# Performance work log

Measured on AMD Instinct MI355X. Metric: run time of the kernel, lower is better.

Reference implementation:

```python
import jax, jax.numpy as jnp
import numpy as np

DIM, HEADS, WH, WW, NPROMPT, NW, BATCH = 384, 12, 7, 7, 5, 64, 32
N = WH * WW + NPROMPT  # 54


def _make_rel_index():
    ch, cw = np.meshgrid(np.arange(WH), np.arange(WW), indexing='ij')
    coords = np.stack([ch, cw]).reshape(2, -1)  # [2, 49]
    rel = coords[:, :, None] - coords[:, None, :]  # [2,49,49]
    rel = rel.transpose(1, 2, 0)
    rel[:, :, 0] += WH - 1
    rel[:, :, 1] += WW - 1
    rel[:, :, 0] *= 2 * WW - 1
    return rel.sum(-1).astype(np.int32)  # [49,49]


def setup_inputs() -> dict:
    key = jax.random.key(0)
    ks = jax.random.split(key, 7)
    B_ = BATCH * NW
    x = jax.random.normal(ks[0], (B_, N, DIM), jnp.float32)
    # 0/-inf style shifted-window mask; random floats exercise the same math
    mask = jnp.where(jax.random.uniform(ks[1], (NW, WH * WW, WH * WW)) > 0.8,
                     jnp.float32(-100.0), jnp.float32(0.0))
    qkv_w = 0.02 * jax.random.normal(ks[2], (3 * DIM, DIM), jnp.float32)
    qkv_b = 0.02 * jax.random.normal(ks[3], (3 * DIM,), jnp.float32)
    proj_w = 0.02 * jax.random.normal(ks[4], (DIM, DIM), jnp.float32)
    proj_b = 0.02 * jax.random.normal(ks[5], (DIM,), jnp.float32)
    rpb_table = 0.02 * jax.random.normal(ks[6], ((2 * WH - 1) * (2 * WW - 1), HEADS), jnp.float32)
    rel_index = jnp.asarray(_make_rel_index())
    return {"x": x, "mask": mask, "qkv_w": qkv_w, "qkv_b": qkv_b,
            "proj_w": proj_w, "proj_b": proj_b, "rpb_table": rpb_table,
            "rel_index": rel_index}


def reference(x, mask, qkv_w, qkv_b, proj_w, proj_b, rpb_table, rel_index):
    B_, n, C = x.shape
    hd = C // HEADS
    scale = hd ** -0.5
    qkv = (x @ qkv_w.T + qkv_b).reshape(B_, n, 3, HEADS, hd)
    qkv = jnp.moveaxis(qkv, 2, 0)  # [3, B_, n, H, hd]
    q, k, v = qkv[0], qkv[1], qkv[2]  # [B_, n, H, hd]
    attn = jnp.einsum('bnhd,bmhd->bhnm', q * scale, k)  # [B_, H, n, n]
    nw2 = WH * WW
    bias = rpb_table[rel_index.reshape(-1)].reshape(nw2, nw2, HEADS)
    bias = jnp.transpose(bias, (2, 0, 1))  # [H, 49, 49]
    bias = jnp.pad(bias, ((0, 0), (NPROMPT, 0), (NPROMPT, 0)))  # [H, n, n]
    attn = attn + bias[None]
    nW = mask.shape[0]
    mask_p = jnp.pad(mask, ((0, 0), (NPROMPT, 0), (NPROMPT, 0)))  # [nW, n, n]
    attn = attn.reshape(B_ // nW, nW, HEADS, n, n) + mask_p[None, :, None]
    attn = jax.nn.softmax(attn.reshape(B_, HEADS, n, n), axis=-1)
    out = jnp.einsum('bhnm,bmhd->bnhd', attn, v).reshape(B_, n, C)
    return out @ proj_w.T + proj_b
```

## Files before the change

kernel.cpp:

```cpp
#include <hip/hip_runtime.h>

#define DIM 384
#define NH 12
#define NT 54
#define NWIN 64
#define MTOT 110592
#define HS ((size_t)MTOT * 32)

typedef __attribute__((ext_vector_type(8))) short short8;
typedef __attribute__((ext_vector_type(4))) float f32x4;

__device__ __forceinline__ unsigned short f2bf(float f) {
  unsigned int u = __float_as_uint(f);
  u += 0x7fffu + ((u >> 16) & 1u);
  return (unsigned short)(u >> 16);
}
__device__ __forceinline__ float bf2f(unsigned short s) {
  return __uint_as_float((unsigned int)s << 16);
}
__device__ __forceinline__ unsigned int cvtpk(float a, float b) {
  unsigned int r;
  asm("v_cvt_pk_bf16_f32 %0, %1, %2" : "=v"(r) : "v"(a), "v"(b));
  return r;
}

__global__ __launch_bounds__(256) void prep2_kernel(
    const float* __restrict__ qkv_w, const float* __restrict__ proj_w,
    const float* __restrict__ mask, const float* __restrict__ rpb,
    const int* __restrict__ rel,
    unsigned short* __restrict__ Wq, unsigned short* __restrict__ Wp,
    unsigned short* __restrict__ bmt) {
  int idx = blockIdx.x * 256 + threadIdx.x;
  if (idx < 1152 * 384) { Wq[idx] = f2bf(qkv_w[idx]); return; }
  idx -= 1152 * 384;
  if (idx < 384 * 384) { Wp[idx] = f2bf(proj_w[idx]); return; }
  idx -= 384 * 384;
  if (idx < NWIN * NH * 64 * 64) {
    int w = idx / (NH * 4096);
    int rem = idx - w * (NH * 4096);
    int h = rem >> 12, r = (rem >> 6) & 63, c = rem & 63;
    float v;
    if (r >= NT || c >= NT) v = -1e30f;
    else if (r >= 5 && c >= 5)
      v = rpb[rel[(r - 5) * 49 + (c - 5)] * NH + h] +
          mask[w * 2401 + (r - 5) * 49 + (c - 5)];
    else v = 0.0f;
    bmt[w * (NH * 4096) + (h << 12) + (c << 6) + r] = f2bf(v);
  }
}

__global__ __launch_bounds__(256) void qkv_gemm4(
    const float* __restrict__ x, const unsigned short* __restrict__ Wq,
    const float* __restrict__ qkv_b,
    unsigned short* __restrict__ Qb, unsigned short* __restrict__ Kb,
    unsigned short* __restrict__ Vb) {
  __shared__ unsigned short As[128][72];
  __shared__ unsigned short Bs[128][72];
  const int s = blockIdx.x;
  const int xcd = s & 7, slot = s >> 3;
  const size_t m0 = (size_t)(xcd * 108 + slot / 9) * 128;
  const int n0 = (slot % 9) * 128;
  const int tid = threadIdx.x;
  const int wv = tid >> 6, ln = tid & 63, g = ln >> 4, lc = ln & 15;
  const int wr = (wv >> 1) * 64, wc = (wv & 1) * 64;
  const int srow = tid >> 3, l8 = tid & 7;

  float4 xa[4], xc[4];
  short8 brg[4];
  f32x4 acc[4][4];
#pragma unroll
  for (int i = 0; i < 4; ++i)
#pragma unroll
    for (int j = 0; j < 4; ++j) acc[i][j] = (f32x4){0.f, 0.f, 0.f, 0.f};

#define QKV_ISSUE(kc_) do {                                              \
    const int k0_ = (kc_) * 64;                                          \
    _Pragma("unroll")                                                    \
    for (int it = 0; it < 4; ++it) {                                     \
      const int r_ = srow + it * 32;                                     \
      const float* ap_ = &x[(m0 + r_) * 384 + k0_ + l8 * 8];             \
      xa[it] = *(const float4*)ap_;                                      \
      xc[it] = *(const float4*)(ap_ + 4);                                \
      brg[it] = *(const short8*)&Wq[(size_t)(n0 + r_) * 384 + k0_ + l8 * 8]; \
    } } while (0)

#define QKV_WRITE() do {                                                 \
    _Pragma("unroll")                                                    \
    for (int it = 0; it < 4; ++it) {                                     \
      const int r_ = srow + it * 32;                                     \
      uint4 u_;                                                          \
      u_.x = cvtpk(xa[it].x, xa[it].y);                                  \
      u_.y = cvtpk(xa[it].z, xa[it].w);                                  \
      u_.z = cvtpk(xc[it].x, xc[it].y);                                  \
      u_.w = cvtpk(xc[it].z, xc[it].w);                                  \
      *(uint4*)&As[r_][l8 * 8] = u_;                                     \
      *(short8*)&Bs[r_][l8 * 8] = brg[it];                               \
    } } while (0)

  QKV_ISSUE(0);
#pragma unroll
  for (int kc = 0; kc < 6; ++kc) {
    if (kc) __syncthreads();
    QKV_WRITE();
    __syncthreads();
    if (kc < 5) QKV_ISSUE(kc + 1);
#pragma unroll
    for (int kk = 0; kk < 2; ++kk) {
      short8 af[4], bfv[4];
#pragma unroll
      for (int ms = 0; ms < 4; ++ms)
        af[ms] = *(const short8*)&As[wr + ms * 16 + lc][kk * 32 + g * 8];
#pragma unroll
      for (int ns = 0; ns < 4; ++ns)
        bfv[ns] = *(const short8*)&Bs[wc + ns * 16 + lc][kk * 32 + g * 8];
#pragma unroll
      for (int ms = 0; ms < 4; ++ms)
#pragma unroll
        for (int ns = 0; ns < 4; ++ns)
          acc[ms][ns] = __builtin_amdgcn_mfma_f32_16x16x32_bf16(
              af[ms], bfv[ns], acc[ms][ns], 0, 0, 0);
    }
  }
#undef QKV_ISSUE
#undef QKV_WRITE

  const int sel = n0 / 384;
  const float factor = (sel == 0) ? 0.17677669529663687f : 1.0f;
  unsigned short* outp = (sel == 0) ? Qb : (sel == 1 ? Kb : Vb);
#pragma unroll
  for (int ns = 0; ns < 4; ++ns) {
    const int n = n0 + wc + ns * 16 + lc;
    const int rl = n - sel * 384;
    const int h = rl >> 5, d = rl & 31;
    const float bias = qkv_b[n];
#pragma unroll
    for (int ms = 0; ms < 4; ++ms) {
      const size_t mrow = m0 + wr + ms * 16 + g * 4;
      const float v0 = (acc[ms][ns][0] + bias) * factor;
      const float v1 = (acc[ms][ns][1] + bias) * factor;
      const float v2 = (acc[ms][ns][2] + bias) * factor;
      const float v3 = (acc[ms][ns][3] + bias) * factor;
      const unsigned int u01 = cvtpk(v0, v1);
      const unsigned int u23 = cvtpk(v2, v3);
      unsigned short* p = &outp[(size_t)h * HS + mrow * 32 + d];
      p[0]  = (unsigned short)(u01 & 0xffffu);
      p[32] = (unsigned short)(u01 >> 16);
      p[64] = (unsigned short)(u23 & 0xffffu);
      p[96] = (unsigned short)(u23 >> 16);
    }
  }
}

__global__ __launch_bounds__(256) void attn2_kernel(
    unsigned short* __restrict__ Qb, const unsigned short* __restrict__ Kb,
    const unsigned short* __restrict__ Vb, const unsigned short* __restrict__ bmt) {
  __shared__ unsigned short Ps[NT][72];
  __shared__ unsigned short vT[32][72];
  const int s = blockIdx.x;
  const int xcd = s & 7, r3 = s >> 3;
  const int h = r3 % 12;
  const int t2 = r3 / 12;
  const int batch = t2 & 31;
  const int w = xcd * 8 + (t2 >> 5);
  const int b = batch * 64 + w;
  const int tid = threadIdx.x;
  const int wv = tid >> 6, ln = tid & 63, g = ln >> 4, lc = ln & 15;
  const int m0 = wv * 16;
  const size_t base = (size_t)b * NT;
  const int arow = (m0 + lc < NT) ? (m0 + lc) : (NT - 1);
  unsigned short* Qh = Qb + (size_t)h * HS;
  const unsigned short* Kh = Kb + (size_t)h * HS;
  const unsigned short* Vh = Vb + (size_t)h * HS;

  for (int i = tid; i < 320; i += 256) {
    int d = i / 10, m = NT + (i - d * 10);
    vT[d][m] = 0;
  }

  const int vr = tid >> 2, vc = (tid & 3) * 8;
  short8 vv;
  if (tid < 216)
    vv = *(const short8*)&Vh[(base + vr) * 32 + vc];

  short8 a = *(const short8*)&Qh[(base + arow) * 32 + g * 8];
  const unsigned short* bmh = &bmt[(size_t)(w * NH + h) << 12];
  const int row0 = m0 + g * 4;
  f32x4 sac[4];
#pragma unroll
  for (int t = 0; t < 4; ++t) {
    const int col = t * 16 + lc;
    const int kr = (col < NT) ? col : (NT - 1);
    short8 kb = *(const short8*)&Kh[(base + kr) * 32 + g * 8];
    uint2 uu = *(const uint2*)&bmh[(col << 6) + row0];
    f32x4 c0;
    c0[0] = bf2f((unsigned short)(uu.x & 0xffffu));
    c0[1] = bf2f((unsigned short)(uu.x >> 16));
    c0[2] = bf2f((unsigned short)(uu.y & 0xffffu));
    c0[3] = bf2f((unsigned short)(uu.y >> 16));
    sac[t] = __builtin_amdgcn_mfma_f32_16x16x32_bf16(a, kb, c0, 0, 0, 0);
  }
  float rmax[4] = {-3.0e38f, -3.0e38f, -3.0e38f, -3.0e38f};
#pragma unroll
  for (int t = 0; t < 4; ++t)
#pragma unroll
    for (int rr = 0; rr < 4; ++rr) rmax[rr] = fmaxf(rmax[rr], sac[t][rr]);
#pragma unroll
  for (int rr = 0; rr < 4; ++rr)
#pragma unroll
    for (int off = 1; off < 16; off <<= 1)
      rmax[rr] = fmaxf(rmax[rr], __shfl_xor(rmax[rr], off));
  float rsum[4] = {0.f, 0.f, 0.f, 0.f};
#pragma unroll
  for (int t = 0; t < 4; ++t)
#pragma unroll
    for (int rr = 0; rr < 4; ++rr) {
      float p = __expf(sac[t][rr] - rmax[rr]);
      sac[t][rr] = p;
      rsum[rr] += p;
    }
#pragma unroll
  for (int rr = 0; rr < 4; ++rr) {
#pragma unroll
    for (int off = 1; off < 16; off <<= 1)
      rsum[rr] += __shfl_xor(rsum[rr], off);
    rsum[rr] = 1.0f / rsum[rr];
  }
#pragma unroll
  for (int t = 0; t < 4; ++t) {
    const int col = t * 16 + lc;
    const unsigned int u01 = cvtpk(sac[t][0] * rsum[0], sac[t][1] * rsum[1]);
    const unsigned int u23 = cvtpk(sac[t][2] * rsum[2], sac[t][3] * rsum[3]);
    if (row0 < NT)     Ps[row0][col]     = (unsigned short)(u01 & 0xffffu);
    if (row0 + 1 < NT) Ps[row0 + 1][col] = (unsigned short)(u01 >> 16);
    if (row0 + 2 < NT) Ps[row0 + 2][col] = (unsigned short)(u23 & 0xffffu);
    if (row0 + 3 < NT) Ps[row0 + 3][col] = (unsigned short)(u23 >> 16);
  }
  if (tid < 216) {
#pragma unroll
    for (int j = 0; j < 8; ++j) vT[vc + j][vr] = (unsigned short)vv[j];
  }
  __syncthreads();
  f32x4 oac[2];
  oac[0] = (f32x4){0.f, 0.f, 0.f, 0.f};
  oac[1] = (f32x4){0.f, 0.f, 0.f, 0.f};
#pragma unroll
  for (int k2 = 0; k2 < 2; ++k2) {
    short8 pa = *(const short8*)&Ps[arow][k2 * 32 + g * 8];
#pragma unroll
    for (int tn = 0; tn < 2; ++tn) {
      short8 vb = *(const short8*)&vT[tn * 16 + lc][k2 * 32 + g * 8];
      oac[tn] = __builtin_amdgcn_mfma_f32_16x16x32_bf16(pa, vb, oac[tn], 0, 0, 0);
    }
  }
#pragma unroll
  for (int tn = 0; tn < 2; ++tn) {
    const int d = tn * 16 + lc;
    const unsigned int u01 = cvtpk(oac[tn][0], oac[tn][1]);
    const unsigned int u23 = cvtpk(oac[tn][2], oac[tn][3]);
    unsigned short* p = &Qh[(base + row0) * 32 + d];
    if (row0 < NT)     p[0]  = (unsigned short)(u01 & 0xffffu);
    if (row0 + 1 < NT) p[32] = (unsigned short)(u01 >> 16);
    if (row0 + 2 < NT) p[64] = (unsigned short)(u23 & 0xffffu);
    if (row0 + 3 < NT) p[96] = (unsigned short)(u23 >> 16);
  }
}

__global__ __launch_bounds__(256) void proj_hmajor(
    const unsigned short* __restrict__ AO, const unsigned short* __restrict__ Wp,
    const float* __restrict__ proj_b, float* __restrict__ out) {
  __shared__ unsigned short As[128][72];
  __shared__ unsigned short Bs[128][72];
  const int s = blockIdx.x;
  const int xcd = s & 7, slot = s >> 3;
  const size_t m0 = (size_t)(xcd * 108 + slot / 3) * 128;
  const int n0 = (slot % 3) * 128;
  const int tid = threadIdx.x;
  const int wv = tid >> 6, ln = tid & 63, g = ln >> 4, lc = ln & 15;
  const int wr = (wv >> 1) * 64, wc = (wv & 1) * 64;
  const int srow = tid >> 3, l8 = tid & 7;

  short8 arg[4], brg[4];
  f32x4 acc[4][4];
#pragma unroll
  for (int i = 0; i < 4; ++i)
#pragma unroll
    for (int j = 0; j < 4; ++j) acc[i][j] = (f32x4){0.f, 0.f, 0.f, 0.f};

#define PRJ_ISSUE(kc_) do {                                              \
    const int kg_ = (kc_) * 64 + l8 * 8;                                 \
    const int hh_ = kg_ >> 5, dd_ = kg_ & 31;                            \
    _Pragma("unroll")                                                    \
    for (int it = 0; it < 4; ++it) {                                     \
      const int r_ = srow + it * 32;                                     \
      arg[it] = *(const short8*)&AO[(size_t)hh_ * HS + (m0 + r_) * 32 + dd_]; \
      brg[it] = *(const short8*)&Wp[(size_t)(n0 + r_) * 384 + kg_];      \
    } } while (0)

#define PRJ_WRITE() do {                                                 \
    _Pragma("unroll")                                                    \
    for (int it = 0; it < 4; ++it) {                                     \
      const int r_ = srow + it * 32;                                     \
      *(short8*)&As[r_][l8 * 8] = arg[it];                               \
      *(short8*)&Bs[r_][l8 * 8] = brg[it];                               \
    } } while (0)

  PRJ_ISSUE(0);
#pragma unroll
  for (int kc = 0; kc < 6; ++kc) {
    if (kc) __syncthreads();
    PRJ_WRITE();
    __syncthreads();
    if (kc < 5) PRJ_ISSUE(kc + 1);
#pragma unroll
    for (int kk = 0; kk < 2; ++kk) {
      short8 af[4], bfv[4];
#pragma unroll
      for (int ms = 0; ms < 4; ++ms)
        af[ms] = *(const short8*)&As[wr + ms * 16 + lc][kk * 32 + g * 8];
#pragma unroll
      for (int ns = 0; ns < 4; ++ns)
        bfv[ns] = *(const short8*)&Bs[wc + ns * 16 + lc][kk * 32 + g * 8];
#pragma unroll
      for (int ms = 0; ms < 4; ++ms)
#pragma unroll
        for (int ns = 0; ns < 4; ++ns)
          acc[ms][ns] = __builtin_amdgcn_mfma_f32_16x16x32_bf16(
              af[ms], bfv[ns], acc[ms][ns], 0, 0, 0);
    }
  }
#undef PRJ_ISSUE
#undef PRJ_WRITE

#pragma unroll
  for (int ns = 0; ns < 4; ++ns) {
    const int n = n0 + wc + ns * 16 + lc;
    const float pb = proj_b[n];
#pragma unroll
    for (int ms = 0; ms < 4; ++ms)
#pragma unroll
      for (int rr = 0; rr < 4; ++rr) {
        const size_t m = m0 + wr + ms * 16 + g * 4 + rr;
        out[m * 384 + n] = acc[ms][ns][rr] + pb;
      }
  }
}

__global__ __launch_bounds__(256) void prep_kernel(
    const float* __restrict__ qkv_w, const float* __restrict__ proj_w,
    const float* __restrict__ mask, const float* __restrict__ rpb,
    const int* __restrict__ rel,
    unsigned short* __restrict__ Wq, unsigned short* __restrict__ Wp,
    float* __restrict__ bias_tab, float* __restrict__ maskp) {
  int idx = blockIdx.x * 256 + threadIdx.x;
  if (idx < 1152 * 384) { Wq[idx] = f2bf(qkv_w[idx]); return; }
  idx -= 1152 * 384;
  if (idx < 384 * 384) { Wp[idx] = f2bf(proj_w[idx]); return; }
  idx -= 384 * 384;
  if (idx < NH * 64 * 64) {
    int h = idx >> 12, r = (idx >> 6) & 63, c = idx & 63;
    float v;
    if (r >= NT || c >= NT) v = -1e30f;
    else if (r >= 5 && c >= 5) v = rpb[rel[(r - 5) * 49 + (c - 5)] * NH + h];
    else v = 0.0f;
    bias_tab[idx] = v;
    return;
  }
  idx -= NH * 64 * 64;
  if (idx < NWIN * 64 * 64) {
    int w = idx >> 12, r = (idx >> 6) & 63, c = idx & 63;
    float v = 0.0f;
    if (r >= 5 && r < NT && c >= 5 && c < NT)
      v = mask[w * 2401 + (r - 5) * 49 + (c - 5)];
    maskp[idx] = v;
  }
}

__global__ __launch_bounds__(256) void fused_attn(
    const float* __restrict__ x, const unsigned short* __restrict__ Wq,
    const float* __restrict__ qkv_b, const float* __restrict__ bias_tab,
    const float* __restrict__ maskp, unsigned short* __restrict__ AO) {
  __shared__ unsigned short xs[NT][392];
  __shared__ unsigned short qs[NT][40];
  __shared__ unsigned short ksm[NT][40];
  __shared__ unsigned short vT[32][72];
  __shared__ unsigned short Ps[NT][72];
  const int b = blockIdx.x;
  const int tid = threadIdx.x;
  const int wv = tid >> 6, ln = tid & 63;
  const int g = ln >> 4, lc = ln & 15;
  const int m0 = wv * 16;
  const int wi = b & 63;
  const float scale = 0.17677669529663687f;
  const float* xb = x + (size_t)b * (NT * DIM);
  for (int i = tid; i < NT * DIM / 4; i += 256) {
    float4 v = ((const float4*)xb)[i];
    int e = i * 4, r = e / DIM, c = e - r * DIM;
    unsigned short* p = &xs[r][c];
    p[0] = f2bf(v.x); p[1] = f2bf(v.y); p[2] = f2bf(v.z); p[3] = f2bf(v.w);
  }
  __syncthreads();
  const int arow = (m0 + lc < NT) ? (m0 + lc) : (NT - 1);
  for (int h = 0; h < NH; ++h) {
    f32x4 acc[6];
#pragma unroll
    for (int t = 0; t < 6; ++t) acc[t] = (f32x4){0.f, 0.f, 0.f, 0.f};
#pragma unroll 2
    for (int kk = 0; kk < 12; ++kk) {
      short8 a = *(const short8*)&xs[arow][kk * 32 + g * 8];
#pragma unroll
      for (int t = 0; t < 6; ++t) {
        const int sel = t >> 1;
        const int wrow = sel * 384 + h * 32 + (t & 1) * 16 + lc;
        short8 bfr = *(const short8*)&Wq[wrow * 384 + kk * 32 + g * 8];
        acc[t] = __builtin_amdgcn_mfma_f32_16x16x32_bf16(a, bfr, acc[t], 0, 0, 0);
      }
    }
#pragma unroll
    for (int t = 0; t < 6; ++t) {
      const int sel = t >> 1;
      const int d = (t & 1) * 16 + lc;
      const float bias = qkv_b[sel * 384 + h * 32 + d];
#pragma unroll
      for (int r = 0; r < 4; ++r) {
        const int m = m0 + g * 4 + r;
        float v = acc[t][r] + bias;
        if (sel == 2) vT[d][m] = f2bf(v);
        else if (m < NT) {
          if (sel == 0) qs[m][d] = f2bf(v * scale);
          else ksm[m][d] = f2bf(v);
        }
      }
    }
    __syncthreads();
    f32x4 sac[4];
    {
      short8 a = *(const short8*)&qs[arow][g * 8];
#pragma unroll
      for (int t = 0; t < 4; ++t) {
        const int kr = (t * 16 + lc < NT) ? (t * 16 + lc) : (NT - 1);
        short8 bfr = *(const short8*)&ksm[kr][g * 8];
        sac[t] = __builtin_amdgcn_mfma_f32_16x16x32_bf16(
            a, bfr, (f32x4){0.f, 0.f, 0.f, 0.f}, 0, 0, 0);
      }
    }
    const float* bt = bias_tab + h * 4096;
    const float* mp = maskp + wi * 4096;
    float sv[4][4];
    float rmax[4];
#pragma unroll
    for (int r = 0; r < 4; ++r) rmax[r] = -3.0e38f;
#pragma unroll
    for (int t = 0; t < 4; ++t) {
      const int col = t * 16 + lc;
#pragma unroll
      for (int r = 0; r < 4; ++r) {
        const int row = m0 + g * 4 + r;
        float s = sac[t][r] + bt[row * 64 + col] + mp[row * 64 + col];
        sv[t][r] = s;
        rmax[r] = fmaxf(rmax[r], s);
      }
    }
#pragma unroll
    for (int r = 0; r < 4; ++r)
#pragma unroll
      for (int off = 1; off < 16; off <<= 1)
        rmax[r] = fmaxf(rmax[r], __shfl_xor(rmax[r], off));
    float rsum[4] = {0.f, 0.f, 0.f, 0.f};
#pragma unroll
    for (int t = 0; t < 4; ++t)
#pragma unroll
      for (int r = 0; r < 4; ++r) {
        float p = __expf(sv[t][r] - rmax[r]);
        sv[t][r] = p;
        rsum[r] += p;
      }
#pragma unroll
    for (int r = 0; r < 4; ++r) {
#pragma unroll
      for (int off = 1; off < 16; off <<= 1)
        rsum[r] += __shfl_xor(rsum[r], off);
      rsum[r] = 1.0f / rsum[r];
    }
#pragma unroll
    for (int t = 0; t < 4; ++t) {
      const int col = t * 16 + lc;
#pragma unroll
      for (int r = 0; r < 4; ++r) {
        const int row = m0 + g * 4 + r;
        if (row < NT) Ps[row][col] = f2bf(sv[t][r] * rsum[r]);
      }
    }
    __syncthreads();
    f32x4 oac[2];
    oac[0] = (f32x4){0.f, 0.f, 0.f, 0.f};
    oac[1] = (f32x4){0.f, 0.f, 0.f, 0.f};
#pragma unroll
    for (int k2 = 0; k2 < 2; ++k2) {
      short8 a = *(const short8*)&Ps[arow][k2 * 32 + g * 8];
#pragma unroll
      for (int tn = 0; tn < 2; ++tn) {
        short8 bfr = *(const short8*)&vT[tn * 16 + lc][k2 * 32 + g * 8];
        oac[tn] = __builtin_amdgcn_mfma_f32_16x16x32_bf16(a, bfr, oac[tn], 0, 0, 0);
      }
    }
    unsigned short* aob = AO + (size_t)b * (NT * DIM) + h * 32;
#pragma unroll
    for (int tn = 0; tn < 2; ++tn) {
      const int d = tn * 16 + lc;
#pragma unroll
      for (int r = 0; r < 4; ++r) {
        const int m = m0 + g * 4 + r;
        if (m < NT) aob[m * DIM + d] = f2bf(oac[tn][r]);
      }
    }
    __syncthreads();
  }
}

__global__ __launch_bounds__(256) void proj_kernel(
    const unsigned short* __restrict__ AO, const unsigned short* __restrict__ Wp,
    const float* __restrict__ proj_b, float* __restrict__ out, int lda) {
  __shared__ unsigned short As[128][72];
  __shared__ unsigned short Bs[128][72];
  const int s = blockIdx.x;
  const int xcd = s & 7, slot = s >> 3;
  const size_t m0 = (size_t)(xcd * 108 + slot / 3) * 128;
  const int n0 = (slot % 3) * 128;
  const int tid = threadIdx.x;
  const int wv = tid >> 6, ln = tid & 63, g = ln >> 4, lc = ln & 15;
  const int wr = (wv >> 1) * 64, wc = (wv & 1) * 64;
  f32x4 acc[4][4];
#pragma unroll
  for (int i = 0; i < 4; ++i)
#pragma unroll
    for (int j = 0; j < 4; ++j) acc[i][j] = (f32x4){0.f, 0.f, 0.f, 0.f};

  const int srow = tid >> 3, l8 = tid & 7;
  for (int kc = 0; kc < 6; ++kc) {
    const int k0 = kc * 64;
#pragma unroll
    for (int it = 0; it < 4; ++it) {
      const int r = srow + it * 32;
      *(short8*)&As[r][l8 * 8] =
          *(const short8*)&AO[(m0 + r) * (size_t)lda + k0 + l8 * 8];
      *(short8*)&Bs[r][l8 * 8] =
          *(const short8*)&Wp[(size_t)(n0 + r) * 384 + k0 + l8 * 8];
    }
    __syncthreads();
#pragma unroll
    for (int kk = 0; kk < 2; ++kk) {
      short8 af[4], bfr[4];
#pragma unroll
      for (int ms = 0; ms < 4; ++ms)
        af[ms] = *(const short8*)&As[wr + ms * 16 + lc][kk * 32 + g * 8];
#pragma unroll
      for (int ns = 0; ns < 4; ++ns)
        bfr[ns] = *(const short8*)&Bs[wc + ns * 16 + lc][kk * 32 + g * 8];
#pragma unroll
      for (int ms = 0; ms < 4; ++ms)
#pragma unroll
        for (int ns = 0; ns < 4; ++ns)
          acc[ms][ns] = __builtin_amdgcn_mfma_f32_16x16x32_bf16(
              af[ms], bfr[ns], acc[ms][ns], 0, 0, 0);
    }
    __syncthreads();
  }
#pragma unroll
  for (int ns = 0; ns < 4; ++ns) {
    const int n = n0 + wc + ns * 16 + lc;
    const float pb = proj_b[n];
#pragma unroll
    for (int ms = 0; ms < 4; ++ms)
#pragma unroll
      for (int rr = 0; rr < 4; ++rr) {
        const size_t m = m0 + wr + ms * 16 + g * 4 + rr;
        out[m * 384 + n] = acc[ms][ns][rr] + pb;
      }
  }
}

extern "C" void kernel_launch(void* const* d_in, const int* in_sizes, int n_in,
                              void* d_out, int out_size, void* d_ws, size_t ws_size,
                              hipStream_t stream) {
  const float* x      = (const float*)d_in[0];
  const float* mask   = (const float*)d_in[1];
  const float* qkv_w  = (const float*)d_in[2];
  const float* qkv_b  = (const float*)d_in[3];
  const float* proj_w = (const float*)d_in[4];
  const float* proj_b = (const float*)d_in[5];
  const float* rpb    = (const float*)d_in[6];
  const int*   rel    = (const int*)d_in[7];
  float* out = (float*)d_out;

  const size_t QKV_ELEMS = (size_t)3 * NH * HS;
  const size_t WQ_ELEMS = 1152 * 384, WP_ELEMS = 384 * 384;
  const size_t BMT_ELEMS = (size_t)NWIN * NH * 4096;
  const size_t need = (QKV_ELEMS + WQ_ELEMS + WP_ELEMS + BMT_ELEMS) * 2;

  if (ws_size >= need) {
    unsigned short* Qb  = (unsigned short*)d_ws;
    unsigned short* Kb  = Qb + NH * HS;
    unsigned short* Vb  = Kb + NH * HS;
    unsigned short* Wq  = Vb + NH * HS;
    unsigned short* Wp  = Wq + WQ_ELEMS;
    unsigned short* bmt = Wp + WP_ELEMS;

    prep2_kernel<<<14592, 256, 0, stream>>>(qkv_w, proj_w, mask, rpb, rel,
                                            Wq, Wp, bmt);
    qkv_gemm4<<<7776, 256, 0, stream>>>(x, Wq, qkv_b, Qb, Kb, Vb);
    attn2_kernel<<<24576, 256, 0, stream>>>(Qb, Kb, Vb, bmt);
    proj_hmajor<<<2592, 256, 0, stream>>>(Qb, Wp, proj_b, out);
  } else {
    unsigned short* Wq = (unsigned short*)d_ws;
    unsigned short* Wp = Wq + 442368;
    float* bias_tab = (float*)(Wp + 147456);
    float* maskp = bias_tab + 12 * 64 * 64;
    unsigned short* AO = (unsigned short*)(maskp + 64 * 64 * 64);
    prep_kernel<<<3520, 256, 0, stream>>>(qkv_w, proj_w, mask, rpb, rel,
                                          Wq, Wp, bias_tab, maskp);
    fused_attn<<<2048, 256, 0, stream>>>(x, Wq, qkv_b, bias_tab, maskp, AO);
    proj_kernel<<<2592, 256, 0, stream>>>(AO, Wp, proj_b, out, 384);
  }
}
```

Measured before the change: 450.6 us.

## Pre-convert x to bf16 and stage GEMM tiles via direct global-to-LDS loads

Measured after the change: 419.0 us. -7.0%, faster.

```diff
diff --git a/kernel.cpp b/kernel.cpp
--- a/kernel.cpp
+++ b/kernel.cpp
@@ -22,6 +22,25 @@
   unsigned int r;
   asm("v_cvt_pk_bf16_f32 %0, %1, %2" : "=v"(r) : "v"(a), "v"(b));
   return r;
+}
+__device__ __forceinline__ void gload16(const unsigned short* g,
+                                        unsigned short* l) {
+  __builtin_amdgcn_global_load_lds(
+      (const __attribute__((address_space(1))) void*)g,
+      (__attribute__((address_space(3))) void*)l, 16, 0, 0);
+}
+
+__global__ __launch_bounds__(256) void convert_x(
+    const float* __restrict__ x, unsigned short* __restrict__ xb) {
+  const size_t i8 = ((size_t)blockIdx.x * 256 + threadIdx.x) * 8;
+  float4 fa = *(const float4*)&x[i8];
+  float4 fb = *(const float4*)&x[i8 + 4];
+  uint4 u;
+  u.x = cvtpk(fa.x, fa.y);
+  u.y = cvtpk(fa.z, fa.w);
+  u.z = cvtpk(fb.x, fb.y);
+  u.w = cvtpk(fb.z, fb.w);
+  *(uint4*)&xb[i8] = u;
 }
 
 __global__ __launch_bounds__(256) void prep2_kernel(
@@ -49,13 +68,13 @@
   }
 }
 
-__global__ __launch_bounds__(256) void qkv_gemm4(
-    const float* __restrict__ x, const unsigned short* __restrict__ Wq,
+__global__ __launch_bounds__(256) void qkv_gemm5(
+    const unsigned short* __restrict__ xb, const unsigned short* __restrict__ Wq,
     const float* __restrict__ qkv_b,
     unsigned short* __restrict__ Qb, unsigned short* __restrict__ Kb,
     unsigned short* __restrict__ Vb) {
-  __shared__ unsigned short As[128][72];
-  __shared__ unsigned short Bs[128][72];
+  __shared__ unsigned short As[128][64];
+  __shared__ unsigned short Bs[128][64];
   const int s = blockIdx.x;
   const int xcd = s & 7, slot = s >> 3;
   const size_t m0 = (size_t)(xcd * 108 + slot / 9) * 128;
@@ -63,56 +82,38 @@
   const int tid = threadIdx.x;
   const int wv = tid >> 6, ln = tid & 63, g = ln >> 4, lc = ln & 15;
   const int wr = (wv >> 1) * 64, wc = (wv & 1) * 64;
-  const int srow = tid >> 3, l8 = tid & 7;
-
-  float4 xa[4], xc[4];
-  short8 brg[4];
+  const int l7 = lc & 7;
+  const int lr8 = ln >> 3;
+  const int sc8 = (((ln & 7) ^ lr8) & 7) * 8;
+
   f32x4 acc[4][4];
 #pragma unroll
   for (int i = 0; i < 4; ++i)
 #pragma unroll
     for (int j = 0; j < 4; ++j) acc[i][j] = (f32x4){0.f, 0.f, 0.f, 0.f};
 
-#define QKV_ISSUE(kc_) do {                                              \
-    const int k0_ = (kc_) * 64;                                          \
-    _Pragma("unroll")                                                    \
-    for (int it = 0; it < 4; ++it) {                                     \
-      const int r_ = srow + it * 32;                                     \
-      const float* ap_ = &x[(m0 + r_) * 384 + k0_ + l8 * 8];             \
-      xa[it] = *(const float4*)ap_;                                      \
-      xc[it] = *(const float4*)(ap_ + 4);                                \
-      brg[it] = *(const short8*)&Wq[(size_t)(n0 + r_) * 384 + k0_ + l8 * 8]; \
-    } } while (0)
-
-#define QKV_WRITE() do {                                                 \
-    _Pragma("unroll")                                                    \
-    for (int it = 0; it < 4; ++it) {                                     \
-      const int r_ = srow + it * 32;                                     \
-      uint4 u_;                                                          \
-      u_.x = cvtpk(xa[it].x, xa[it].y);                                  \
-      u_.y = cvtpk(xa[it].z, xa[it].w);                                  \
-      u_.z = cvtpk(xc[it].x, xc[it].y);                                  \
-      u_.w = cvtpk(xc[it].z, xc[it].w);                                  \
-      *(uint4*)&As[r_][l8 * 8] = u_;                                     \
-      *(short8*)&Bs[r_][l8 * 8] = brg[it];                               \
-    } } while (0)
-
-  QKV_ISSUE(0);
 #pragma unroll
   for (int kc = 0; kc < 6; ++kc) {
+    const int k0 = kc * 64;
     if (kc) __syncthreads();
-    QKV_WRITE();
+#pragma unroll
+    for (int it = 0; it < 4; ++it) {
+      const int r0 = wv * 32 + it * 8;
+      const int r = r0 + lr8;
+      gload16(&xb[(m0 + r) * 384 + k0 + sc8], &As[r0][0]);
+      gload16(&Wq[(size_t)(n0 + r) * 384 + k0 + sc8], &Bs[r0][0]);
+    }
     __syncthreads();
-    if (kc < 5) QKV_ISSUE(kc + 1);
 #pragma unroll
     for (int kk = 0; kk < 2; ++kk) {
+      const int cix = (((kk * 4 + g) ^ l7)) * 8;
       short8 af[4], bfv[4];
 #pragma unroll
       for (int ms = 0; ms < 4; ++ms)
-        af[ms] = *(const short8*)&As[wr + ms * 16 + lc][kk * 32 + g * 8];
+        af[ms] = *(const short8*)&As[wr + ms * 16 + lc][cix];
 #pragma unroll
       for (int ns = 0; ns < 4; ++ns)
-        bfv[ns] = *(const short8*)&Bs[wc + ns * 16 + lc][kk * 32 + g * 8];
+        bfv[ns] = *(const short8*)&Bs[wc + ns * 16 + lc][cix];
 #pragma unroll
       for (int ms = 0; ms < 4; ++ms)
 #pragma unroll
@@ -121,8 +122,6 @@
               af[ms], bfv[ns], acc[ms][ns], 0, 0, 0);
     }
   }
-#undef QKV_ISSUE
-#undef QKV_WRITE
 
   const int sel = n0 / 384;
   const float factor = (sel == 0) ? 0.17677669529663687f : 1.0f;
@@ -268,8 +267,8 @@
 __global__ __launch_bounds__(256) void proj_hmajor(
     const unsigned short* __restrict__ AO, const unsigned short* __restrict__ Wp,
     const float* __restrict__ proj_b, float* __restrict__ out) {
-  __shared__ unsigned short As[128][72];
-  __shared__ unsigned short Bs[128][72];
+  __shared__ unsigned short As[128][64];
+  __shared__ unsigned short Bs[128][64];
   const int s = blockIdx.x;
   const int xcd = s & 7, slot = s >> 3;
   const size_t m0 = (size_t)(xcd * 108 + slot / 3) * 128;
@@ -277,49 +276,39 @@
   const int tid = threadIdx.x;
   const int wv = tid >> 6, ln = tid & 63, g = ln >> 4, lc = ln & 15;
   const int wr = (wv >> 1) * 64, wc = (wv & 1) * 64;
-  const int srow = tid >> 3, l8 = tid & 7;
-
-  short8 arg[4], brg[4];
+  const int l7 = lc & 7;
+  const int lr8 = ln >> 3;
+  const int sc8 = (((ln & 7) ^ lr8) & 7) * 8;
+
   f32x4 acc[4][4];
 #pragma unroll
   for (int i = 0; i < 4; ++i)
 #pragma unroll
     for (int j = 0; j < 4; ++j) acc[i][j] = (f32x4){0.f, 0.f, 0.f, 0.f};
 
-#define PRJ_ISSUE(kc_) do {                                              \
-    const int kg_ = (kc_) * 64 + l8 * 8;                                 \
-    const int hh_ = kg_ >> 5, dd_ = kg_ & 31;                            \
-    _Pragma("unroll")                                                    \
-    for (int it = 0; it < 4; ++it) {                                     \
-      const int r_ = srow + it * 32;                                     \
-      arg[it] = *(const short8*)&AO[(size_t)hh_ * HS + (m0 + r_) * 32 + dd_]; \
-      brg[it] = *(const short8*)&Wp[(size_t)(n0 + r_) * 384 + kg_];      \
-    } } while (0)
-
-#define PRJ_WRITE() do {                                                 \
-    _Pragma("unroll")                                                    \
-    for (int it = 0; it < 4; ++it) {                                     \
-      const int r_ = srow + it * 32;                                     \
-      *(short8*)&As[r_][l8 * 8] = arg[it];                               \
-      *(short8*)&Bs[r_][l8 * 8] = brg[it];                               \
-    } } while (0)
-
-  PRJ_ISSUE(0);
 #pragma unroll
   for (int kc = 0; kc < 6; ++kc) {
+    const int kg = kc * 64 + sc8;
+    const int hh = kg >> 5, dd = kg & 31;
     if (kc) __syncthreads();
-    PRJ_WRITE();
+#pragma unroll
+    for (int it = 0; it < 4; ++it) {
+      const int r0 = wv * 32 + it * 8;
+      const int r = r0 + lr8;
+      gload16(&AO[(size_t)hh * HS + (m0 + r) * 32 + dd], &As[r0][0]);
+      gload16(&Wp[(size_t)(n0 + r) * 384 + kg], &Bs[r0][0]);
+    }
     __syncthreads();
-    if (kc < 5) PRJ_ISSUE(kc + 1);
 #pragma unroll
     for (int kk = 0; kk < 2; ++kk) {
+      const int cix = (((kk * 4 + g) ^ l7)) * 8;
       short8 af[4], bfv[4];
 #pragma unroll
       for (int ms = 0; ms < 4; ++ms)
-        af[ms] = *(const short8*)&As[wr + ms * 16 + lc][kk * 32 + g * 8];
+        af[ms] = *(const short8*)&As[wr + ms * 16 + lc][cix];
 #pragma unroll
       for (int ns = 0; ns < 4; ++ns)
-        bfv[ns] = *(const short8*)&Bs[wc + ns * 16 + lc][kk * 32 + g * 8];
+        bfv[ns] = *(const short8*)&Bs[wc + ns * 16 + lc][cix];
 #pragma unroll
       for (int ms = 0; ms < 4; ++ms)
 #pragma unroll
@@ -328,8 +317,6 @@
               af[ms], bfv[ns], acc[ms][ns], 0, 0, 0);
     }
   }
-#undef PRJ_ISSUE
-#undef PRJ_WRITE
 
 #pragma unroll
   for (int ns = 0; ns < 4; ++ns) {
@@ -604,10 +591,12 @@
     unsigned short* Wq  = Vb + NH * HS;
     unsigned short* Wp  = Wq + WQ_ELEMS;
     unsigned short* bmt = Wp + WP_ELEMS;
-
+    unsigned short* xb = (unsigned short*)d_out;
+
+    convert_x<<<20736, 256, 0, stream>>>(x, xb);
     prep2_kernel<<<14592, 256, 0, stream>>>(qkv_w, proj_w, mask, rpb, rel,
                                             Wq, Wp, bmt);
-    qkv_gemm4<<<7776, 256, 0, stream>>>(x, Wq, qkv_b, Qb, Kb, Vb);
+    qkv_gemm5<<<7776, 256, 0, stream>>>(xb, Wq, qkv_b, Qb, Kb, Vb);
     attn2_kernel<<<24576, 256, 0, stream>>>(Qb, Kb, Vb, bmt);
     proj_hmajor<<<2592, 256, 0, stream>>>(Qb, Wp, proj_b, out);
   } else {
```
